# Kernel tuning notes

Hardware: AMD Instinct MI355X
Metric: run time of the kernel (lower is better)

## Reference

```python
import jax, jax.numpy as jnp
import numpy as np

NUM_HEADS = 8
N_CHUNKS = 4


def _chunk_bounds(n, chunks):
    # replicate torch.chunk: chunk size = ceil(n/chunks), last chunk smaller
    cs = -(-n // chunks)
    return [min(i * cs, n) for i in range(chunks + 1)]


def setup_inputs() -> dict:
    key = jax.random.key(0)
    ks = jax.random.split(key, 9)
    dim, N, B = 512, 289, 256
    C = dim // 2
    H, d = NUM_HEADS, C // NUM_HEADS
    return {
        "x1": jax.random.normal(ks[0], (B, N, dim), jnp.float32),
        "x2": jax.random.normal(ks[1], (B, N, dim), jnp.float32),
        "W_reduce": jax.random.normal(ks[2], (dim, C), jnp.float32) * 0.02,
        "W_qkv": jax.random.normal(ks[3], (C, 3 * C), jnp.float32) * 0.02,
        "W_proj": jax.random.normal(ks[4], (C, dim), jnp.float32) * 0.02,
        "b_proj": jnp.zeros((dim,), jnp.float32),
        "w_ds": 1.0 + 0.02 * jax.random.normal(ks[5], (H, d), jnp.float32),
        "w_uds": 1.0 + 0.02 * jax.random.normal(ks[6], (H, d), jnp.float32),
        "b_uds": jnp.zeros((H, d), jnp.float32),
    }


def _branch(x, W_reduce, W_qkv, W_proj, b_proj, w_ds, w_uds, b_uds, use_ds):
    xr = x @ W_reduce                       # [B, N, C]
    B, N, C = xr.shape
    H = NUM_HEADS
    d = C // H
    scale = d ** -0.5
    qkv = (xr @ W_qkv).reshape(B, N, 3, H, d).transpose(2, 0, 3, 1, 4)  # [3,B,H,N,d]
    q, k, v = qkv[0], qkv[1], qkv[2]
    bounds = _chunk_bounds(N, N_CHUNKS)
    outs = []
    for i in range(N_CHUNKS):               # fixed 4-way chunking, per original
        s, e = bounds[i], bounds[i + 1]
        qc, kc, vc = q[:, :, s:e], k[:, :, s:e], v[:, :, s:e]
        if use_ds:
            # Distributive: learned per-head diagonal metric on head_dim, scale folded in
            attn = jnp.einsum('bhnd,bhmd->bhnm', qc * w_ds[None, :, None, :], kc) * scale
        else:
            # UnDistributive: learned per-head affine on q and k, then scaled dot-product
            qc = qc * w_uds[None, :, None, :] + b_uds[None, :, None, :]
            kc = kc * w_uds[None, :, None, :] + b_uds[None, :, None, :]
            attn = jnp.einsum('bhnd,bhmd->bhnm', qc, kc) * scale
        attn = jax.nn.softmax(attn, axis=-1)
        outs.append(jnp.einsum('bhnm,bhmd->bnhd', attn, vc))  # (attn @ v).transpose(1,2)
    o = jnp.concatenate(outs, axis=1).reshape(B, N, C)
    return o @ W_proj + b_proj


def reference(x1, x2, W_reduce, W_qkv, W_proj, b_proj, w_ds, w_uds, b_uds):
    y1 = _branch(x1, W_reduce, W_qkv, W_proj, b_proj, w_ds, w_uds, b_uds, use_ds=True)
    y2 = _branch(x2, W_reduce, W_qkv, W_proj, b_proj, w_ds, w_uds, b_uds, use_ds=False)
    return (y1, y2)
```

## Files before the change

### kernel.cpp

```cpp
#include <hip/hip_runtime.h>

typedef __bf16 bf16;
typedef bf16 bf16x4 __attribute__((ext_vector_type(4)));
typedef bf16 bf16x8 __attribute__((ext_vector_type(8)));
typedef float f32x4 __attribute__((ext_vector_type(4)));

#define LOG2E 1.4426950408889634f

__device__ __forceinline__ f32x4 mfma16(bf16x8 a, bf16x8 b, f32x4 c) {
    return __builtin_amdgcn_mfma_f32_16x16x32_bf16(a, b, c, 0, 0, 0);
}

__device__ __forceinline__ void async16(const void* g, void* l) {
    __builtin_amdgcn_global_load_lds(
        (const __attribute__((address_space(1))) void*)g,
        (__attribute__((address_space(3))) void*)l, 16, 0, 0);
}

__global__ __launch_bounds__(256) void prep_w(
    const float* __restrict__ Wr, const float* __restrict__ Wq,
    const float* __restrict__ w_ds, const float* __restrict__ w_uds,
    const float* __restrict__ b_uds,
    bf16* __restrict__ W1t, bf16* __restrict__ W2t, float* __restrict__ bias) {
    __shared__ float wq[256][17];
    const int t = threadIdx.x;
    const int k0 = blockIdx.x * 64, n0 = blockIdx.y * 16, z = blockIdx.z;
#pragma unroll
    for (int i = 0; i < 16; i++) {
        int c = i * 16 + (t >> 4);
        wq[c][t & 15] = Wq[c * 768 + n0 + (t & 15)];
    }
    __syncthreads();
    const int j = t & 15, n = n0 + j;
    const float rs = 0.17677669529663687f;
    float scale, bv;
    if (z == 0) {
        scale = (n < 256) ? w_ds[n] * rs : 1.f; bv = 0.f;
    } else if (n < 256) {
        scale = w_uds[n] * rs; bv = b_uds[n] * rs;
    } else if (n < 512) {
        scale = w_uds[n - 256]; bv = b_uds[n - 256];
    } else {
        scale = 1.f; bv = 0.f;
    }
    bf16* Wt = z ? W2t : W1t;
#pragma unroll 1
    for (int i = 0; i < 4; i++) {
        int k = k0 + (t >> 4) * 4 + i;
        float acc = 0.f;
        for (int c = 0; c < 256; c++) acc = fmaf(Wr[k * 256 + c], wq[c][j], acc);
        Wt[n * 512 + k] = (bf16)(acc * scale);
    }
    if (blockIdx.x == 0 && (t >> 4) == 0) bias[z * 768 + n] = bv;
}

__global__ void prep_wp(const float* __restrict__ Wp, bf16* __restrict__ Wpt) {
    const int n = blockIdx.x, k = threadIdx.x;
    Wpt[n * 256 + k] = (bf16)Wp[k * 512 + n];
}

__global__ __launch_bounds__(256) void xcast(const float* __restrict__ X1,
                                             const float* __restrict__ X2,
                                             bf16* __restrict__ O1,
                                             bf16* __restrict__ O2) {
    const float* X = blockIdx.y ? X2 : X1;
    bf16* O = blockIdx.y ? O2 : O1;
    const long total = 37879808;
    const long stride = (long)gridDim.x * 256 * 8;
    for (long i = ((long)blockIdx.x * 256 + threadIdx.x) * 8; i < total; i += stride) {
        float4 a = *(const float4*)&X[i];
        float4 b = *(const float4*)&X[i + 4];
        bf16x8 w = {(bf16)a.x, (bf16)a.y, (bf16)a.z, (bf16)a.w,
                    (bf16)b.x, (bf16)b.y, (bf16)b.z, (bf16)b.w};
        *(bf16x8*)&O[i] = w;
    }
}

__global__ __launch_bounds__(256, 4) void gemm_qkv(
    const bf16* __restrict__ X, const bf16* __restrict__ Wt,
    const float* __restrict__ biasp, bf16* __restrict__ Out) {
    __shared__ __attribute__((aligned(16))) bf16 As[2][128 * 32];
    __shared__ __attribute__((aligned(16))) bf16 Bs[2][128 * 32];
    const int tid = threadIdx.x;
    const int lane = tid & 63, wave = tid >> 6;
    const int ln = lane & 15, quad = lane >> 4;
    const int bn = blockIdx.x * 128, bm = blockIdx.y * 128;
    const int wm = (wave & 1) * 64, wn = (wave >> 1) * 64;
    f32x4 acc[4][4] = {};
    float bi[4];
#pragma unroll
    for (int nt = 0; nt < 4; nt++) bi[nt] = biasp[bn + wn + nt * 16 + ln];
    const int arow = bm + wave * 32 + (lane >> 2);
    const int brow = bn + wave * 32 + (lane >> 2);
    const int c0 = (lane & 3) * 8;
    bf16* as0 = &As[0][(wave * 32) * 32];
    bf16* as1 = &As[0][(wave * 32 + 16) * 32];
    bf16* bs0 = &Bs[0][(wave * 32) * 32];
    bf16* bs1 = &Bs[0][(wave * 32 + 16) * 32];
    const int bufstride = 128 * 32;

    async16(&X[arow * 512 + c0], as0);
    async16(&X[(arow + 16) * 512 + c0], as1);
    async16(&Wt[brow * 512 + c0], bs0);
    async16(&Wt[(brow + 16) * 512 + c0], bs1);
    __syncthreads();

    int cur = 0;
#pragma unroll 1
    for (int kb = 0; kb < 512; kb += 32) {
        const int kn = kb + 32;
        const int nxt = cur ^ 1;
        if (kn < 512) {
            async16(&X[arow * 512 + kn + c0], as0 + nxt * bufstride);
            async16(&X[(arow + 16) * 512 + kn + c0], as1 + nxt * bufstride);
            async16(&Wt[brow * 512 + kn + c0], bs0 + nxt * bufstride);
            async16(&Wt[(brow + 16) * 512 + kn + c0], bs1 + nxt * bufstride);
        }
        bf16x8 a[4], b[4];
#pragma unroll
        for (int mt = 0; mt < 4; mt++)
            a[mt] = *(const bf16x8*)&As[cur][(wm + mt * 16 + ln) * 32 + quad * 8];
#pragma unroll
        for (int nt = 0; nt < 4; nt++)
            b[nt] = *(const bf16x8*)&Bs[cur][(wn + nt * 16 + ln) * 32 + quad * 8];
#pragma unroll
        for (int mt = 0; mt < 4; mt++)
#pragma unroll
            for (int nt = 0; nt < 4; nt++)
                acc[mt][nt] = mfma16(a[mt], b[nt], acc[mt][nt]);
        __syncthreads();
        cur = nxt;
    }
#pragma unroll
    for (int mt = 0; mt < 4; mt++)
#pragma unroll
        for (int nt = 0; nt < 4; nt++) {
            int col = bn + wn + nt * 16 + ln;
#pragma unroll
            for (int r = 0; r < 4; r++) {
                int row = bm + wm + mt * 16 + quad * 4 + r;
                Out[row * 768 + col] = (bf16)(acc[mt][nt][r] + bi[nt]);
            }
        }
}

__global__ __launch_bounds__(256, 4) void gemm_proj(
    const bf16* __restrict__ A, const bf16* __restrict__ Wt,
    const float* __restrict__ bp, float* __restrict__ Y) {
    __shared__ __attribute__((aligned(16))) bf16 As[2][128 * 32];
    __shared__ __attribute__((aligned(16))) bf16 Bs[2][128 * 32];
    const int tid = threadIdx.x;
    const int lane = tid & 63, wave = tid >> 6;
    const int ln = lane & 15, quad = lane >> 4;
    const int bn = blockIdx.x * 128, bm = blockIdx.y * 128;
    const int wm = (wave & 1) * 64, wn = (wave >> 1) * 64;
    f32x4 acc[4][4] = {};
    float bi[4];
#pragma unroll
    for (int nt = 0; nt < 4; nt++) bi[nt] = bp[bn + wn + nt * 16 + ln];
    const int arow = bm + wave * 32 + (lane >> 2);
    const int brow = bn + wave * 32 + (lane >> 2);
    const int c0 = (lane & 3) * 8;
    bf16* as0 = &As[0][(wave * 32) * 32];
    bf16* as1 = &As[0][(wave * 32 + 16) * 32];
    bf16* bs0 = &Bs[0][(wave * 32) * 32];
    bf16* bs1 = &Bs[0][(wave * 32 + 16) * 32];
    const int bufstride = 128 * 32;

    async16(&A[arow * 256 + c0], as0);
    async16(&A[(arow + 16) * 256 + c0], as1);
    async16(&Wt[brow * 256 + c0], bs0);
    async16(&Wt[(brow + 16) * 256 + c0], bs1);
    __syncthreads();

    int cur = 0;
#pragma unroll 1
    for (int kb = 0; kb < 256; kb += 32) {
        const int kn = kb + 32;
        const int nxt = cur ^ 1;
        if (kn < 256) {
            async16(&A[arow * 256 + kn + c0], as0 + nxt * bufstride);
            async16(&A[(arow + 16) * 256 + kn + c0], as1 + nxt * bufstride);
            async16(&Wt[brow * 256 + kn + c0], bs0 + nxt * bufstride);
            async16(&Wt[(brow + 16) * 256 + kn + c0], bs1 + nxt * bufstride);
        }
        bf16x8 a[4], b[4];
#pragma unroll
        for (int mt = 0; mt < 4; mt++)
            a[mt] = *(const bf16x8*)&As[cur][(wm + mt * 16 + ln) * 32 + quad * 8];
#pragma unroll
        for (int nt = 0; nt < 4; nt++)
            b[nt] = *(const bf16x8*)&Bs[cur][(wn + nt * 16 + ln) * 32 + quad * 8];
#pragma unroll
        for (int mt = 0; mt < 4; mt++)
#pragma unroll
            for (int nt = 0; nt < 4; nt++)
                acc[mt][nt] = mfma16(a[mt], b[nt], acc[mt][nt]);
        __syncthreads();
        cur = nxt;
    }
#pragma unroll
    for (int mt = 0; mt < 4; mt++)
#pragma unroll
        for (int nt = 0; nt < 4; nt++) {
            int col = bn + wn + nt * 16 + ln;
#pragma unroll
            for (int r = 0; r < 4; r++) {
                int row = bm + wm + mt * 16 + quad * 4 + r;
                Y[row * 512 + col] = acc[mt][nt][r] + bi[nt];
            }
        }
}

__global__ __launch_bounds__(256) void attn(const bf16* __restrict__ QKV,
                                            bf16* __restrict__ O) {
    __shared__ __attribute__((aligned(16))) bf16 vT[4][32 * 104];
    __shared__ __attribute__((aligned(16))) bf16 P[4][16 * 104];
    const int tid = threadIdx.x;
    const int lane = tid & 63, wave = tid >> 6;
    const int ln = lane & 15, quad = lane >> 4;
    const int chunk = blockIdx.x, b = blockIdx.y;
    const int s = chunk * 73;
    const int mc = min(289 - s, 73);
    const int rowbase = b * 289 + s;
    bf16* vTw = &vT[wave][0];
    bf16* Pw = &P[wave][0];
    const f32x4 zero4 = {0.f, 0.f, 0.f, 0.f};

    {
        bf16x4 z = {(bf16)0.f, (bf16)0.f, (bf16)0.f, (bf16)0.f};
        *(bf16x4*)&Pw[(lane >> 2) * 104 + 80 + (lane & 3) * 4] = z;
    }

#pragma unroll 1
    for (int hi = 0; hi < 2; hi++) {
        const int h = wave + hi * 4;
        const int cq = h * 32, ck = 256 + h * 32, cv = 512 + h * 32;

#pragma unroll
        for (int p5 = 0; p5 < 6; p5++) {
            int m = p5 * 16 + (lane >> 2);
            int mr = min(m, mc - 1);
            bf16x8 v8 = *(const bf16x8*)&QKV[(rowbase + mr) * 768 + cv + (lane & 3) * 8];
            int d0 = (lane & 3) * 8;
#pragma unroll
            for (int j = 0; j < 8; j++) vTw[(d0 + j) * 104 + m] = v8[j];
        }
        bf16x8 kf[5];
#pragma unroll
        for (int mt = 0; mt < 5; mt++) {
            int mr = min(mt * 16 + ln, mc - 1);
            kf[mt] = *(const bf16x8*)&QKV[(rowbase + mr) * 768 + ck + quad * 8];
        }
        bf16x8 vf[2][3];
#pragma unroll
        for (int dt = 0; dt < 2; dt++)
#pragma unroll
            for (int mk = 0; mk < 3; mk++)
                vf[dt][mk] = *(const bf16x8*)&vTw[(dt * 16 + ln) * 104 + mk * 32 + quad * 8];

#pragma unroll 1
        for (int nt = 0; nt < 5; nt++) {
            int qr = min(nt * 16 + ln, mc - 1);
            bf16x8 qf = *(const bf16x8*)&QKV[(rowbase + qr) * 768 + cq + quad * 8];
            f32x4 S[5];
#pragma unroll
            for (int mt = 0; mt < 5; mt++) S[mt] = mfma16(qf, kf[mt], zero4);
#pragma unroll
            for (int mt = 0; mt < 5; mt++)
                if (mt * 16 + ln >= mc) {
                    S[mt][0] = -1e30f; S[mt][1] = -1e30f;
                    S[mt][2] = -1e30f; S[mt][3] = -1e30f;
                }
            float mxv[4], sm[4];
#pragma unroll
            for (int r = 0; r < 4; r++) {
                float m0 = S[0][r];
#pragma unroll
                for (int mt = 1; mt < 5; mt++) m0 = fmaxf(m0, S[mt][r]);
                m0 = fmaxf(m0, __shfl_xor(m0, 1));
                m0 = fmaxf(m0, __shfl_xor(m0, 2));
                m0 = fmaxf(m0, __shfl_xor(m0, 4));
                m0 = fmaxf(m0, __shfl_xor(m0, 8));
                mxv[r] = m0;
                sm[r] = 0.f;
            }
#pragma unroll
            for (int mt = 0; mt < 5; mt++)
#pragma unroll
                for (int r = 0; r < 4; r++) {
                    float p = exp2f((S[mt][r] - mxv[r]) * LOG2E);
                    sm[r] += p;
                    Pw[(quad * 4 + r) * 104 + mt * 16 + ln] = (bf16)p;
                }
#pragma unroll
            for (int r = 0; r < 4; r++) {
                float t = sm[r];
                t += __shfl_xor(t, 1);
                t += __shfl_xor(t, 2);
                t += __shfl_xor(t, 4);
                t += __shfl_xor(t, 8);
                sm[r] = 1.0f / t;
            }
            f32x4 o0 = zero4, o1 = zero4;
#pragma unroll
            for (int mk = 0; mk < 3; mk++) {
                bf16x8 pa = *(const bf16x8*)&Pw[ln * 104 + mk * 32 + quad * 8];
                o0 = mfma16(pa, vf[0][mk], o0);
                o1 = mfma16(pa, vf[1][mk], o1);
            }
#pragma unroll
            for (int r = 0; r < 4; r++) {
                int nl = nt * 16 + quad * 4 + r;
                if (nl < mc) {
                    int orow = (rowbase + nl) * 256 + h * 32;
                    O[orow + ln] = (bf16)(o0[r] * sm[r]);
                    O[orow + 16 + ln] = (bf16)(o1[r] * sm[r]);
                }
            }
        }
    }
}

extern "C" void kernel_launch(void* const* d_in, const int* in_sizes, int n_in,
                              void* d_out, int out_size, void* d_ws, size_t ws_size,
                              hipStream_t stream) {
    (void)in_sizes; (void)n_in; (void)out_size; (void)ws_size;
    const float* x1 = (const float*)d_in[0];
    const float* x2 = (const float*)d_in[1];
    const float* Wr = (const float*)d_in[2];
    const float* Wq = (const float*)d_in[3];
    const float* Wp = (const float*)d_in[4];
    const float* bp = (const float*)d_in[5];
    const float* w_ds = (const float*)d_in[6];
    const float* w_uds = (const float*)d_in[7];
    const float* b_uds = (const float*)d_in[8];

    char* ws = (char*)d_ws;
    bf16* W1t = (bf16*)(ws);
    bf16* W2t = (bf16*)(ws + 786432);
    bf16* Wpt = (bf16*)(ws + 1572864);
    float* bias = (float*)(ws + 1835008);
    bf16* ob = (bf16*)(ws + 1841152);
    float* out = (float*)d_out;
    char* outc = (char*)d_out;
    bf16* Xb1 = (bf16*)(outc);
    bf16* Xb2 = (bf16*)(outc + 75759616);
    bf16* qkv = (bf16*)(outc + 151519232);

    prep_w<<<dim3(8, 48, 2), 256, 0, stream>>>(Wr, Wq, w_ds, w_uds, b_uds, W1t, W2t, bias);
    prep_wp<<<dim3(512), 256, 0, stream>>>(Wp, Wpt);
    xcast<<<dim3(2048, 2), 256, 0, stream>>>(x1, x2, Xb1, Xb2);

    gemm_qkv<<<dim3(6, 578), 256, 0, stream>>>(Xb1, W1t, bias, qkv);
    attn<<<dim3(4, 256), 256, 0, stream>>>(qkv, ob);
    gemm_qkv<<<dim3(6, 578), 256, 0, stream>>>(Xb2, W2t, bias + 768, qkv);
    gemm_proj<<<dim3(4, 578), 256, 0, stream>>>(ob, Wpt, bp, out);
    attn<<<dim3(4, 256), 256, 0, stream>>>(qkv, ob);
    gemm_proj<<<dim3(4, 578), 256, 0, stream>>>(ob, Wpt, bp, out + (size_t)37879808);
}
```

Measured before the change: 902.0 us.

## Replace QKV and projection GEMMs with 256x256-tile, 8-wave pipelined shared kernel

Both GEMM kernels are replaced by one templated 256x256 tile GEMM using 8 waves and 512 threads. It uses double-buffered async global-to-LDS loads with an XOR-swizzled LDS layout and interleaves prefetch with MFMA phases, split by raw s_barrier and vmcnt waits plus s_setprio. The larger tile raises data reuse per LDS load and the swizzle aims to reduce bank conflicts. In exchange it uses 128KB of LDS and more accumulator registers, which lowers occupancy, and relies on hand-placed waitcnt ordering that is fragile.

```diff
diff --git a/kernel.cpp b/kernel.cpp
--- a/kernel.cpp
+++ b/kernel.cpp
@@ -76,140 +76,132 @@
     }
 }
 
-__global__ __launch_bounds__(256, 4) void gemm_qkv(
-    const bf16* __restrict__ X, const bf16* __restrict__ Wt,
-    const float* __restrict__ biasp, bf16* __restrict__ Out) {
-    __shared__ __attribute__((aligned(16))) bf16 As[2][128 * 32];
-    __shared__ __attribute__((aligned(16))) bf16 Bs[2][128 * 32];
+template <int KT, int KS, int LDO, int OUTF32>
+__device__ __forceinline__ void gemm8(const bf16* __restrict__ A,
+                                      const bf16* __restrict__ B,
+                                      const float* __restrict__ biasp,
+                                      void* __restrict__ OutP, bf16* Lf) {
     const int tid = threadIdx.x;
     const int lane = tid & 63, wave = tid >> 6;
     const int ln = lane & 15, quad = lane >> 4;
-    const int bn = blockIdx.x * 128, bm = blockIdx.y * 128;
-    const int wm = (wave & 1) * 64, wn = (wave >> 1) * 64;
-    f32x4 acc[4][4] = {};
+    const int wm = wave >> 2, wn = wave & 3;
+    const int bn = blockIdx.x * 256, bm = blockIdx.y * 256;
+    f32x4 acc[8][4] = {};
     float bi[4];
 #pragma unroll
-    for (int nt = 0; nt < 4; nt++) bi[nt] = biasp[bn + wn + nt * 16 + ln];
-    const int arow = bm + wave * 32 + (lane >> 2);
-    const int brow = bn + wave * 32 + (lane >> 2);
-    const int c0 = (lane & 3) * 8;
-    bf16* as0 = &As[0][(wave * 32) * 32];
-    bf16* as1 = &As[0][(wave * 32 + 16) * 32];
-    bf16* bs0 = &Bs[0][(wave * 32) * 32];
-    bf16* bs1 = &Bs[0][(wave * 32 + 16) * 32];
-    const int bufstride = 128 * 32;
-
-    async16(&X[arow * 512 + c0], as0);
-    async16(&X[(arow + 16) * 512 + c0], as1);
-    async16(&Wt[brow * 512 + c0], bs0);
-    async16(&Wt[(brow + 16) * 512 + c0], bs1);
-    __syncthreads();
-
-    int cur = 0;
+    for (int nr = 0; nr < 4; nr++) bi[nr] = biasp[bn + wn * 64 + nr * 16 + ln];
+
+    const int srow = tid >> 2;
+    const int schunk = ((tid & 3) ^ ((tid >> 3) & 3)) * 8;
+    const int rq = (quad ^ ((ln >> 1) & 3)) * 8;
+    const int abase = (wm * 128 + ln) * 32 + rq;
+    const int bbase = 16384 + (wn * 64 + ln) * 32 + rq;
+
+    auto stA = [&](int buf, int kk, int h, int kb) {
+        async16(&A[(long)(bm + h * 128 + srow) * KS + kb + kk * 32 + schunk],
+                Lf + buf * 32768 + kk * 8192 + (h * 128 + wave * 16) * 32);
+    };
+    auto stB = [&](int buf, int kk, int h, int kb) {
+        async16(&B[(long)(bn + h * 128 + srow) * KS + kb + kk * 32 + schunk],
+                Lf + buf * 32768 + 16384 + kk * 8192 + (h * 128 + wave * 16) * 32);
+    };
+
+    stA(0, 0, 0, 0); stA(0, 0, 1, 0); stB(0, 0, 0, 0); stB(0, 0, 1, 0);
+    stA(0, 1, 0, 0); stA(0, 1, 1, 0); stB(0, 1, 0, 0); stB(0, 1, 1, 0);
+
 #pragma unroll 1
-    for (int kb = 0; kb < 512; kb += 32) {
-        const int kn = kb + 32;
-        const int nxt = cur ^ 1;
-        if (kn < 512) {
-            async16(&X[arow * 512 + kn + c0], as0 + nxt * bufstride);
-            async16(&X[(arow + 16) * 512 + kn + c0], as1 + nxt * bufstride);
-            async16(&Wt[brow * 512 + kn + c0], bs0 + nxt * bufstride);
-            async16(&Wt[(brow + 16) * 512 + kn + c0], bs1 + nxt * bufstride);
+    for (int kt = 0; kt < KT; ++kt) {
+        const int cb = kt & 1, nb = cb ^ 1, kb = (kt + 1) * 64;
+        const bool pf = (kt + 1) < KT;
+        const int aoff = cb * 32768 + abase;
+        const int boff = cb * 32768 + bbase;
+        bf16x8 aF[4], bF[4], aG[4];
+        asm volatile("s_waitcnt vmcnt(4)" ::: "memory");
+        __builtin_amdgcn_s_barrier();
+        asm volatile("" ::: "memory");
+#pragma unroll
+        for (int i = 0; i < 4; i++) aF[i] = *(const bf16x8*)&Lf[aoff + i * 512];
+#pragma unroll
+        for (int i = 0; i < 4; i++) bF[i] = *(const bf16x8*)&Lf[boff + i * 512];
+        if (pf) { stA(nb, 0, 0, kb); stA(nb, 0, 1, kb); }
+        __builtin_amdgcn_s_setprio(1);
+#pragma unroll
+        for (int i = 0; i < 4; i++)
+#pragma unroll
+            for (int j = 0; j < 4; j++) acc[i][j] = mfma16(aF[i], bF[j], acc[i][j]);
+        __builtin_amdgcn_s_setprio(0);
+        asm volatile("" ::: "memory");
+        __builtin_amdgcn_s_barrier();
+        asm volatile("" ::: "memory");
+#pragma unroll
+        for (int i = 0; i < 4; i++) aG[i] = *(const bf16x8*)&Lf[aoff + (i + 4) * 512];
+        if (pf) { stB(nb, 0, 0, kb); stB(nb, 0, 1, kb); }
+        __builtin_amdgcn_s_setprio(1);
+#pragma unroll
+        for (int i = 0; i < 4; i++)
+#pragma unroll
+            for (int j = 0; j < 4; j++) acc[i + 4][j] = mfma16(aG[i], bF[j], acc[i + 4][j]);
+        __builtin_amdgcn_s_setprio(0);
+        if (pf) asm volatile("s_waitcnt vmcnt(4)" ::: "memory");
+        else    asm volatile("s_waitcnt vmcnt(0)" ::: "memory");
+        __builtin_amdgcn_s_barrier();
+        asm volatile("" ::: "memory");
+#pragma unroll
+        for (int i = 0; i < 4; i++) aF[i] = *(const bf16x8*)&Lf[aoff + 8192 + i * 512];
+#pragma unroll
+        for (int i = 0; i < 4; i++) bF[i] = *(const bf16x8*)&Lf[boff + 8192 + i * 512];
+        if (pf) { stA(nb, 1, 0, kb); stA(nb, 1, 1, kb); }
+        __builtin_amdgcn_s_setprio(1);
+#pragma unroll
+        for (int i = 0; i < 4; i++)
+#pragma unroll
+            for (int j = 0; j < 4; j++) acc[i][j] = mfma16(aF[i], bF[j], acc[i][j]);
+        __builtin_amdgcn_s_setprio(0);
+        asm volatile("" ::: "memory");
+        __builtin_amdgcn_s_barrier();
+        asm volatile("" ::: "memory");
+#pragma unroll
+        for (int i = 0; i < 4; i++) aG[i] = *(const bf16x8*)&Lf[aoff + 8192 + (i + 4) * 512];
+        if (pf) { stB(nb, 1, 0, kb); stB(nb, 1, 1, kb); }
+        __builtin_amdgcn_s_setprio(1);
+#pragma unroll
+        for (int i = 0; i < 4; i++)
+#pragma unroll
+            for (int j = 0; j < 4; j++) acc[i + 4][j] = mfma16(aG[i], bF[j], acc[i + 4][j]);
+        __builtin_amdgcn_s_setprio(0);
+    }
+#pragma unroll
+    for (int i = 0; i < 8; i++)
+#pragma unroll
+        for (int j = 0; j < 4; j++) {
+            const int col = bn + wn * 64 + j * 16 + ln;
+            const long row0 = bm + wm * 128 + i * 16 + quad * 4;
+            if (OUTF32) {
+                float* Y = (float*)OutP;
+#pragma unroll
+                for (int r = 0; r < 4; r++)
+                    Y[(row0 + r) * LDO + col] = acc[i][j][r] + bi[j];
+            } else {
+                bf16* Y = (bf16*)OutP;
+#pragma unroll
+                for (int r = 0; r < 4; r++)
+                    Y[(row0 + r) * LDO + col] = (bf16)(acc[i][j][r] + bi[j]);
+            }
         }
-        bf16x8 a[4], b[4];
-#pragma unroll
-        for (int mt = 0; mt < 4; mt++)
-            a[mt] = *(const bf16x8*)&As[cur][(wm + mt * 16 + ln) * 32 + quad * 8];
-#pragma unroll
-        for (int nt = 0; nt < 4; nt++)
-            b[nt] = *(const bf16x8*)&Bs[cur][(wn + nt * 16 + ln) * 32 + quad * 8];
-#pragma unroll
-        for (int mt = 0; mt < 4; mt++)
-#pragma unroll
-            for (int nt = 0; nt < 4; nt++)
-                acc[mt][nt] = mfma16(a[mt], b[nt], acc[mt][nt]);
-        __syncthreads();
-        cur = nxt;
-    }
-#pragma unroll
-    for (int mt = 0; mt < 4; mt++)
-#pragma unroll
-        for (int nt = 0; nt < 4; nt++) {
-            int col = bn + wn + nt * 16 + ln;
-#pragma unroll
-            for (int r = 0; r < 4; r++) {
-                int row = bm + wm + mt * 16 + quad * 4 + r;
-                Out[row * 768 + col] = (bf16)(acc[mt][nt][r] + bi[nt]);
-            }
-        }
-}
-
-__global__ __launch_bounds__(256, 4) void gemm_proj(
-    const bf16* __restrict__ A, const bf16* __restrict__ Wt,
+}
+
+__global__ __launch_bounds__(512, 2) void gemm_qkv8(
+    const bf16* __restrict__ X, const bf16* __restrict__ Wt,
+    const float* __restrict__ biasp, bf16* __restrict__ Out) {
+    __shared__ __attribute__((aligned(16))) bf16 L[65536];
+    gemm8<8, 512, 768, 0>(X, Wt, biasp, Out, L);
+}
+
+__global__ __launch_bounds__(512, 2) void gemm_proj8(
+    const bf16* __restrict__ Ain, const bf16* __restrict__ Wpt,
     const float* __restrict__ bp, float* __restrict__ Y) {
-    __shared__ __attribute__((aligned(16))) bf16 As[2][128 * 32];
-    __shared__ __attribute__((aligned(16))) bf16 Bs[2][128 * 32];
-    const int tid = threadIdx.x;
-    const int lane = tid & 63, wave = tid >> 6;
-    const int ln = lane & 15, quad = lane >> 4;
-    const int bn = blockIdx.x * 128, bm = blockIdx.y * 128;
-    const int wm = (wave & 1) * 64, wn = (wave >> 1) * 64;
-    f32x4 acc[4][4] = {};
-    float bi[4];
-#pragma unroll
-    for (int nt = 0; nt < 4; nt++) bi[nt] = bp[bn + wn + nt * 16 + ln];
-    const int arow = bm + wave * 32 + (lane >> 2);
-    const int brow = bn + wave * 32 + (lane >> 2);
-    const int c0 = (lane & 3) * 8;
-    bf16* as0 = &As[0][(wave * 32) * 32];
-    bf16* as1 = &As[0][(wave * 32 + 16) * 32];
-    bf16* bs0 = &Bs[0][(wave * 32) * 32];
-    bf16* bs1 = &Bs[0][(wave * 32 + 16) * 32];
-    const int bufstride = 128 * 32;
-
-    async16(&A[arow * 256 + c0], as0);
-    async16(&A[(arow + 16) * 256 + c0], as1);
-    async16(&Wt[brow * 256 + c0], bs0);
-    async16(&Wt[(brow + 16) * 256 + c0], bs1);
-    __syncthreads();
-
-    int cur = 0;
-#pragma unroll 1
-    for (int kb = 0; kb < 256; kb += 32) {
-        const int kn = kb + 32;
-        const int nxt = cur ^ 1;
-        if (kn < 256) {
-            async16(&A[arow * 256 + kn + c0], as0 + nxt * bufstride);
-            async16(&A[(arow + 16) * 256 + kn + c0], as1 + nxt * bufstride);
-            async16(&Wt[brow * 256 + kn + c0], bs0 + nxt * bufstride);
-            async16(&Wt[(brow + 16) * 256 + kn + c0], bs1 + nxt * bufstride);
-        }
-        bf16x8 a[4], b[4];
-#pragma unroll
-        for (int mt = 0; mt < 4; mt++)
-            a[mt] = *(const bf16x8*)&As[cur][(wm + mt * 16 + ln) * 32 + quad * 8];
-#pragma unroll
-        for (int nt = 0; nt < 4; nt++)
-            b[nt] = *(const bf16x8*)&Bs[cur][(wn + nt * 16 + ln) * 32 + quad * 8];
-#pragma unroll
-        for (int mt = 0; mt < 4; mt++)
-#pragma unroll
-            for (int nt = 0; nt < 4; nt++)
-                acc[mt][nt] = mfma16(a[mt], b[nt], acc[mt][nt]);
-        __syncthreads();
-        cur = nxt;
-    }
-#pragma unroll
-    for (int mt = 0; mt < 4; mt++)
-#pragma unroll
-        for (int nt = 0; nt < 4; nt++) {
-            int col = bn + wn + nt * 16 + ln;
-#pragma unroll
-            for (int r = 0; r < 4; r++) {
-                int row = bm + wm + mt * 16 + quad * 4 + r;
-                Y[row * 512 + col] = acc[mt][nt][r] + bi[nt];
-            }
-        }
+    __shared__ __attribute__((aligned(16))) bf16 L[65536];
+    gemm8<4, 256, 512, 1>(Ain, Wpt, bp, Y, L);
 }
 
 __global__ __launch_bounds__(256) void attn(const bf16* __restrict__ QKV,
@@ -352,10 +344,10 @@
     prep_wp<<<dim3(512), 256, 0, stream>>>(Wp, Wpt);
     xcast<<<dim3(2048, 2), 256, 0, stream>>>(x1, x2, Xb1, Xb2);
 
-    gemm_qkv<<<dim3(6, 578), 256, 0, stream>>>(Xb1, W1t, bias, qkv);
+    gemm_qkv8<<<dim3(3, 289), 512, 0, stream>>>(Xb1, W1t, bias, qkv);
     attn<<<dim3(4, 256), 256, 0, stream>>>(qkv, ob);
-    gemm_qkv<<<dim3(6, 578), 256, 0, stream>>>(Xb2, W2t, bias + 768, qkv);
-    gemm_proj<<<dim3(4, 578), 256, 0, stream>>>(ob, Wpt, bp, out);
+    gemm_qkv8<<<dim3(3, 289), 512, 0, stream>>>(Xb2, W2t, bias + 768, qkv);
+    gemm_proj8<<<dim3(2, 289), 512, 0, stream>>>(ob, Wpt, bp, out);
     attn<<<dim3(4, 256), 256, 0, stream>>>(qkv, ob);
-    gemm_proj<<<dim3(4, 578), 256, 0, stream>>>(ob, Wpt, bp, out + (size_t)37879808);
-}
+    gemm_proj8<<<dim3(2, 289), 512, 0, stream>>>(ob, Wpt, bp, out + (size_t)37879808);
+}
```

Result: no change. 897.0 us (-0.5%).
